# Kernel tuning notes

Hardware: AMD Instinct MI355X
Metric: run time of the kernel (lower is better)

Reference implementation:

```python
import jax, jax.numpy as jnp
import numpy as np

BS, C_IN, CTX, TGT = 2, 8, 1024, 96
D_MODEL, N_HEADS, D_FF, N_LAYERS = 256, 16, 1024, 4
PF, SF, PC, SC = 8, 4, 32, 16
NF = (CTX + SF - PF) // SF + 1   # 256 fine patches (incl. end-pad)
NC = (CTX + SC - PC) // SC + 1   # 64 coarse patches
TOTAL = NF + NC                  # 320
EPS = 1e-5
DK = D_MODEL // N_HEADS
SCALE = DK ** -0.5


def _patchify(z, plen, stride):
    # ReplicationPad1d((0, stride)) then unfold -> (bs, c, n_patches, plen)
    pad = jnp.broadcast_to(z[..., -1:], z.shape[:-1] + (stride,))
    zp = jnp.concatenate([z, pad], axis=-1)
    n = (zp.shape[-1] - plen) // stride + 1
    idx = np.arange(n)[:, None] * stride + np.arange(plen)[None, :]
    return zp[..., idx]


def _layernorm(x, s, b):
    m = x.mean(-1, keepdims=True)
    v = jnp.var(x, axis=-1, keepdims=True)
    return (x - m) * jax.lax.rsqrt(v + EPS) * s + b


def setup_inputs() -> dict:
    key = jax.random.key(0)
    ks = jax.random.split(key, 16)
    g = lambda k, shape: jax.random.normal(k, shape, jnp.float32) * 0.02
    return {
        "z": jax.random.normal(ks[0], (BS, C_IN, CTX), jnp.float32),
        "revin_w": jnp.ones((C_IN,), jnp.float32),
        "revin_b": jnp.zeros((C_IN,), jnp.float32),
        "Wf": g(ks[1], (PF, D_MODEL)), "bf": jnp.zeros((D_MODEL,), jnp.float32),
        "Wc": g(ks[2], (PC, D_MODEL)), "bc": jnp.zeros((D_MODEL,), jnp.float32),
        "W_pos": jax.random.uniform(ks[3], (TOTAL, D_MODEL), jnp.float32, -0.02, 0.02),
        "WQ": g(ks[4], (N_LAYERS, D_MODEL, D_MODEL)), "bQ": jnp.zeros((N_LAYERS, D_MODEL), jnp.float32),
        "WK": g(ks[5], (N_LAYERS, D_MODEL, D_MODEL)), "bK": jnp.zeros((N_LAYERS, D_MODEL), jnp.float32),
        "WV": g(ks[6], (N_LAYERS, D_MODEL, D_MODEL)), "bV": jnp.zeros((N_LAYERS, D_MODEL), jnp.float32),
        "WO": g(ks[7], (N_LAYERS, D_MODEL, D_MODEL)), "bO": jnp.zeros((N_LAYERS, D_MODEL), jnp.float32),
        "ln1_s": jnp.ones((N_LAYERS, D_MODEL), jnp.float32), "ln1_b": jnp.zeros((N_LAYERS, D_MODEL), jnp.float32),
        "ln2_s": jnp.ones((N_LAYERS, D_MODEL), jnp.float32), "ln2_b": jnp.zeros((N_LAYERS, D_MODEL), jnp.float32),
        "F1": g(ks[8], (N_LAYERS, D_MODEL, D_FF)), "c1": jnp.zeros((N_LAYERS, D_FF), jnp.float32),
        "F2": g(ks[9], (N_LAYERS, D_FF, D_MODEL)), "c2": jnp.zeros((N_LAYERS, D_MODEL), jnp.float32),
        "Wh": g(ks[10], (D_MODEL * TOTAL, TGT)), "bh": jnp.zeros((TGT,), jnp.float32),
    }


def reference(z, revin_w, revin_b, Wf, bf, Wc, bc, W_pos, WQ, bQ, WK, bK, WV, bV,
              WO, bO, ln1_s, ln1_b, ln2_s, ln2_b, F1, c1, F2, c2, Wh, bh):
    # RevIN norm over the time axis (last axis of (bs, c, T))
    mean = z.mean(-1, keepdims=True)
    std = jnp.sqrt(jnp.var(z, axis=-1, keepdims=True) + EPS)
    zn = (z - mean) / std * revin_w[None, :, None] + revin_b[None, :, None]

    # dual-scale patch embedding
    x_fine = _patchify(zn, PF, SF) @ Wf + bf      # (bs, c, NF, d)
    x_coarse = _patchify(zn, PC, SC) @ Wc + bc    # (bs, c, NC, d)
    x = jnp.concatenate([x_fine, x_coarse], axis=2)  # (bs, c, TOTAL, d)

    u = x.reshape(BS * C_IN, TOTAL, D_MODEL) + W_pos  # (B, S, d), B=bs*c

    # residual-score transformer encoder (post-norm)
    prev = None
    for l in range(N_LAYERS):
        q = (u @ WQ[l] + bQ[l]).reshape(-1, TOTAL, N_HEADS, DK).transpose(0, 2, 1, 3)
        k = (u @ WK[l] + bK[l]).reshape(-1, TOTAL, N_HEADS, DK).transpose(0, 2, 1, 3)
        v = (u @ WV[l] + bV[l]).reshape(-1, TOTAL, N_HEADS, DK).transpose(0, 2, 1, 3)
        s = jnp.einsum('bhqd,bhkd->bhqk', q, k) * SCALE
        if prev is not None:
            s = s + prev
        w = jax.nn.softmax(s, axis=-1)
        o = jnp.einsum('bhqk,bhkd->bhqd', w, v).transpose(0, 2, 1, 3).reshape(-1, TOTAL, D_MODEL)
        o = o @ WO[l] + bO[l]
        u = _layernorm(u + o, ln1_s[l], ln1_b[l])
        h = jax.nn.gelu(u @ F1[l] + c1[l], approximate=False) @ F2[l] + c2[l]
        u = _layernorm(u + h, ln2_s[l], ln2_b[l])
        prev = s

    # head: (bs, c, TOTAL, d) -> permute -> flatten(d, TOTAL) -> linear
    zz = u.reshape(BS, C_IN, TOTAL, D_MODEL).transpose(0, 1, 3, 2).reshape(BS, C_IN, D_MODEL * TOTAL)
    out = zz @ Wh + bh  # (bs, c, TGT)

    # RevIN denorm
    out = (out - revin_b[None, :, None]) / (revin_w[None, :, None] + EPS * EPS) * std + mean
    return out
```

## Files before the change

kernel.cpp:

```cpp
#include <hip/hip_runtime.h>
#include <math.h>

typedef unsigned short ushort;
typedef unsigned int uint;
typedef __attribute__((ext_vector_type(8))) short short8;
typedef __attribute__((ext_vector_type(4))) float f32x4;
typedef __attribute__((ext_vector_type(4))) ushort us4;

constexpr int BS = 2, C_IN = 8, CTX = 1024, TGT = 96;
constexpr int DM = 256, NH = 16, DFF = 1024, NL = 4;
constexpr int NF = 256, TOTAL = 320;
constexpr int NB = 16;
constexpr int DK = 16;
constexpr float EPS = 1e-5f;
constexpr float SCALE = 0.25f;
constexpr int KHEAD = DM * TOTAL;
constexpr int M = NB * TOTAL;

__device__ __forceinline__ ushort f2b(float x) {
    uint u = __float_as_uint(x);
    u += 0x7fff + ((u >> 16) & 1);
    return (ushort)(u >> 16);
}
__device__ __forceinline__ float bu2f(ushort x) { return __uint_as_float(((uint)x) << 16); }
__device__ __forceinline__ uint pack2(float a, float b) { return (uint)f2b(a) | ((uint)f2b(b) << 16); }

typedef __attribute__((address_space(3))) uint lds_u32;
typedef const __attribute__((address_space(1))) uint glb_u32;
__device__ __forceinline__ void ldst16(const void* g, void* l) {
    __builtin_amdgcn_global_load_lds((glb_u32*)g, (lds_u32*)l, 16, 0, 0);
}

#define PIPE_BARRIER() asm volatile("s_waitcnt vmcnt(0)\n\ts_barrier" ::: "memory")

__global__ __launch_bounds__(256) void k_prep(
        const float* __restrict__ WQ, const float* __restrict__ WK,
        const float* __restrict__ WV, const float* __restrict__ WO,
        const float* __restrict__ F1, const float* __restrict__ F2,
        const float* __restrict__ Wh,
        ushort* __restrict__ Wtqkv, ushort* __restrict__ WtO,
        ushort* __restrict__ Ft1, ushort* __restrict__ Ft2,
        ushort* __restrict__ WhT2,
        const float* __restrict__ z, const float* __restrict__ rw,
        const float* __restrict__ rb,
        const float* __restrict__ Wf, const float* __restrict__ bfv,
        const float* __restrict__ Wc, const float* __restrict__ bcv,
        const float* __restrict__ Wpos, ushort* __restrict__ u,
        const float* __restrict__ bhv, float* __restrict__ outp,
        float* __restrict__ scalef) {
    __shared__ __align__(16) ushort tile[64 * 98];
    __shared__ float szn[CTX];
    __shared__ float red1[4], red2[4];
    int i = blockIdx.x, tid = threadIdx.x;

    if (i < 768) {
        const float* src; ushort* dst; int lsrc, ldst_, r0, c0;
        if (i < 256) {
            int mat = i >> 4, l = mat >> 2, w = mat & 3;
            src = (w == 0 ? WQ : (w == 1 ? WK : (w == 2 ? WV : WO))) + l * 65536;
            dst = (w < 3) ? (Wtqkv + (size_t)l * 768 * 256 + w * 65536)
                          : (WtO + (size_t)l * 65536);
            lsrc = 256; ldst_ = 256; r0 = ((i >> 2) & 3) * 64; c0 = (i & 3) * 64;
        } else if (i < 512) {
            int j = i - 256, l = j >> 6, t = j & 63;
            src = F1 + (size_t)l * 262144; dst = Ft1 + (size_t)l * 262144;
            lsrc = 1024; ldst_ = 256; r0 = (t >> 4) * 64; c0 = (t & 15) * 64;
        } else {
            int j = i - 512, l = j >> 6, t = j & 63;
            src = F2 + (size_t)l * 262144; dst = Ft2 + (size_t)l * 262144;
            lsrc = 256; ldst_ = 1024; r0 = (t >> 2) * 64; c0 = (t & 3) * 64;
        }
#pragma unroll
        for (int it = 0; it < 4; it++) {
            int fid = it * 256 + tid;
            int fr = fid >> 4, fc = fid & 15;
            f32x4 v = *(const f32x4*)&src[(size_t)(r0 + fr) * lsrc + c0 + fc * 4];
            ushort* tr = &tile[fr * 66];
            tr[fc * 4 + 0] = f2b(v[0]); tr[fc * 4 + 1] = f2b(v[1]);
            tr[fc * 4 + 2] = f2b(v[2]); tr[fc * 4 + 3] = f2b(v[3]);
        }
        __syncthreads();
#pragma unroll
        for (int it = 0; it < 4; it++) {
            int sid = it * 256 + tid;
            int cr = sid >> 4, cc = sid & 15;
            us4 v = (us4){ tile[(cc * 4 + 0) * 66 + cr], tile[(cc * 4 + 1) * 66 + cr],
                           tile[(cc * 4 + 2) * 66 + cr], tile[(cc * 4 + 3) * 66 + cr] };
            *(us4*)&dst[(size_t)(c0 + cr) * ldst_ + r0 + cc * 4] = v;
        }
    } else if (i < 2048) {
        int j = i - 768;
        int pp = j >> 2, d0 = (j & 3) * 64;
#pragma unroll
        for (int it = 0; it < 6; it++) {
            int fid = it * 256 + tid;
            int fr = fid / 24, fc = fid % 24;
            f32x4 v = *(const f32x4*)&Wh[((size_t)(d0 + fr) * 320 + pp) * 96 + fc * 4];
            ushort* tr = &tile[fr * 98];
            tr[fc * 4 + 0] = f2b(v[0]); tr[fc * 4 + 1] = f2b(v[1]);
            tr[fc * 4 + 2] = f2b(v[2]); tr[fc * 4 + 3] = f2b(v[3]);
        }
        __syncthreads();
#pragma unroll
        for (int it = 0; it < 6; it++) {
            int sid = it * 256 + tid;
            int tr = sid >> 4, dc = sid & 15;
            us4 v = (us4){ tile[(dc * 4 + 0) * 98 + tr], tile[(dc * 4 + 1) * 98 + tr],
                           tile[(dc * 4 + 2) * 98 + tr], tile[(dc * 4 + 3) * 98 + tr] };
            *(us4*)&WhT2[(size_t)tr * KHEAD + pp * 256 + d0 + dc * 4] = v;
        }
    } else {
        int j = i - 2048;
        int bc = j / 80, pb = j % 80;
        int wave = tid >> 6, lane = tid & 63;
        f32x4 zv = *(const f32x4*)&z[bc * CTX + tid * 4];
        float s1 = zv[0] + zv[1] + zv[2] + zv[3];
        float s2 = zv[0] * zv[0] + zv[1] * zv[1] + zv[2] * zv[2] + zv[3] * zv[3];
#pragma unroll
        for (int off = 1; off < 64; off <<= 1) {
            s1 += __shfl_xor(s1, off);
            s2 += __shfl_xor(s2, off);
        }
        if (lane == 0) { red1[wave] = s1; red2[wave] = s2; }
        __syncthreads();
        s1 = red1[0] + red1[1] + red1[2] + red1[3];
        s2 = red2[0] + red2[1] + red2[2] + red2[3];
        float m = s1 * (1.0f / CTX);
        float var = s2 * (1.0f / CTX) - m * m;
        float sd = sqrtf(var + EPS);
        int c = bc & 7;
        float w = rw[c], bb = rb[c];
        float inv_sd_w = w / sd;
#pragma unroll
        for (int k = 0; k < 4; k++) szn[tid * 4 + k] = (zv[k] - m) * inv_sd_w + bb;
        if (pb == 0) {
            if (tid < TGT) outp[bc * TGT + tid] = (bhv[tid] - bb) / (w + EPS * EPS) * sd + m;
            if (tid == 0) scalef[bc] = sd / (w + EPS * EPS);
        }
        __syncthreads();
#pragma unroll
        for (int pi = 0; pi < 4; pi++) {
            int p = pb * 4 + pi, d = tid;
            float acc;
            if (p < NF) {
                acc = bfv[d];
                int base = p * 4;
#pragma unroll
                for (int q = 0; q < 8; q++)
                    acc += szn[min(base + q, CTX - 1)] * Wf[q * DM + d];
            } else {
                acc = bcv[d];
                int base = (p - NF) * 16;
#pragma unroll
                for (int q = 0; q < 32; q++)
                    acc += szn[min(base + q, CTX - 1)] * Wc[q * DM + d];
            }
            acc += Wpos[p * DM + d];
            u[((size_t)bc * TOTAL + p) * DM + d] = f2b(acc);
        }
    }
}

template <int GELU, int QKV>
__global__ __launch_bounds__(256) void k_gemm_mfma(const ushort* __restrict__ A,
                                                   const ushort* __restrict__ Wt,
                                                   const float* __restrict__ b0,
                                                   const float* __restrict__ b1,
                                                   const float* __restrict__ b2,
                                                   ushort* __restrict__ C,
                                                   ushort* __restrict__ C2,
                                                   int Mm, int N, int K) {
    __shared__ ushort As[2][64][32];
    __shared__ ushort Bs[2][64][32];
    int tid = threadIdx.x;
    int wave = tid >> 6, lane = tid & 63;
    int quad = lane >> 4, l16 = lane & 15;
    int m0 = blockIdx.y * 64, n0 = blockIdx.x * 64;

    f32x4 acc[4];
#pragma unroll
    for (int nt = 0; nt < 4; nt++) acc[nt] = (f32x4){0.f, 0.f, 0.f, 0.f};

    int srow = wave * 16 + (lane >> 2);
    int sc = (lane & 3) ^ ((srow >> 1) & 3);
    const ushort* Ag = &A[(size_t)(m0 + srow) * K + sc * 8];
    const ushort* Bg = &Wt[(size_t)(n0 + srow) * K + sc * 8];
    int rchunk = (quad ^ ((l16 >> 1) & 3)) * 8;

    ldst16(Ag, &As[0][wave * 16][0]);
    ldst16(Bg, &Bs[0][wave * 16][0]);
    PIPE_BARRIER();

    int nstep = K >> 5;
    int cur = 0;
    for (int t = 0; t < nstep; t++) {
        if (t + 1 < nstep) {
            ldst16(Ag + (t + 1) * 32, &As[cur ^ 1][wave * 16][0]);
            ldst16(Bg + (t + 1) * 32, &Bs[cur ^ 1][wave * 16][0]);
        }
        short8 af = *(const short8*)&As[cur][wave * 16 + l16][rchunk];
#pragma unroll
        for (int nt = 0; nt < 4; nt++) {
            short8 bf = *(const short8*)&Bs[cur][nt * 16 + l16][rchunk];
            acc[nt] = __builtin_amdgcn_mfma_f32_16x16x32_bf16(af, bf, acc[nt], 0, 0, 0);
        }
        PIPE_BARRIER();
        cur ^= 1;
    }
#pragma unroll
    for (int nt = 0; nt < 4; nt++) {
        int col = n0 + nt * 16 + l16;
        float bi;
        if (QKV) {
            int bs = (n0 + nt * 16) >> 8;
            const float* bp = bs == 0 ? b0 : (bs == 1 ? b1 : b2);
            bi = bp[col & 255];
        } else {
            bi = b0[col];
        }
#pragma unroll
        for (int r = 0; r < 4; r++) {
            int rowm = m0 + wave * 16 + quad * 4 + r;
            float vv = acc[nt][r] + bi;
            if (GELU) vv = vv * 0.5f * (1.0f + erff(vv * 0.70710678118f));
            if (QKV) {
                int bs = col >> 8;
                int c = col & 255, hh = c >> 4, d = c & 15;
                int bb = rowm / 320, j = rowm - bb * 320;
                size_t plane = (size_t)hh * (M * DK) + (size_t)bb * (TOTAL * DK);
                if (bs == 0) {
                    C[plane + (size_t)j * DK + d] = f2b(vv);
                } else if (bs == 1) {
                    int off = (((j >> 4) * 2 + (d >> 3)) * 16 + (j & 15)) * 8 + (d & 7);
                    C[(size_t)M * DM + plane + off] = f2b(vv);
                } else {
                    int off = ((j >> 5) * 4 + ((j & 15) >> 2)) * 128 +
                              (((j >> 4) & 1) << 2) + (j & 3) + d * 8;
                    C2[plane + off] = f2b(vv);
                }
            } else {
                C[(size_t)rowm * N + col] = f2b(vv);
            }
        }
    }
}

__global__ __launch_bounds__(256) void k_block(const ushort* __restrict__ ax,
                                               const ushort* __restrict__ WtO,
                                               const float* __restrict__ bO,
                                               const float* __restrict__ ln1s,
                                               const float* __restrict__ ln1b,
                                               const ushort* __restrict__ F1t,
                                               const ushort* __restrict__ F2t,
                                               const float* __restrict__ c1v,
                                               const float* __restrict__ c2v,
                                               const float* __restrict__ ln2s,
                                               const float* __restrict__ ln2b,
                                               ushort* __restrict__ u) {
    __shared__ ushort As[2][16][32];
    __shared__ ushort Bs[2][256][32];
    __shared__ __align__(16) ushort Au[16][264];
    __shared__ __align__(16) ushort Hs[16][264];
    __shared__ float ps1[16][4], ps2[16][4];
    int tid = threadIdx.x;
    int wave = tid >> 6, lane = tid & 63;
    int quad = lane >> 4, l16 = lane & 15;
    int m0 = blockIdx.x * 16;

    int brow = wave * 16 + (lane >> 2);
    int bsw = (lane & 3) ^ ((brow >> 1) & 3);
    int ar = lane >> 2;
    int ac = (lane & 3) ^ ((ar >> 1) & 3);
    int rchunk = (quad ^ ((l16 >> 1) & 3)) * 8;

    {
        f32x4 acc[4];
#pragma unroll
        for (int nt = 0; nt < 4; nt++) acc[nt] = (f32x4){0.f, 0.f, 0.f, 0.f};
        const ushort* Ag = &ax[(size_t)(m0 + ar) * 256 + ac * 8];
        const ushort* Bg = &WtO[(size_t)brow * 256 + bsw * 8];

        if (tid < 64) ldst16(Ag, &As[0][0][0]);
#pragma unroll
        for (int i = 0; i < 4; i++) ldst16(Bg + (size_t)i * 64 * 256, &Bs[0][i * 64 + wave * 16][0]);
        PIPE_BARRIER();
        int cur = 0;
        for (int t = 0; t < 8; t++) {
            if (t + 1 < 8) {
                if (tid < 64) ldst16(Ag + (t + 1) * 32, &As[cur ^ 1][0][0]);
#pragma unroll
                for (int i = 0; i < 4; i++)
                    ldst16(Bg + (size_t)i * 64 * 256 + (t + 1) * 32, &Bs[cur ^ 1][i * 64 + wave * 16][0]);
            }
            short8 af = *(const short8*)&As[cur][l16][rchunk];
#pragma unroll
            for (int nt = 0; nt < 4; nt++) {
                short8 bf = *(const short8*)&Bs[cur][wave * 64 + nt * 16 + l16][rchunk];
                acc[nt] = __builtin_amdgcn_mfma_f32_16x16x32_bf16(af, bf, acc[nt], 0, 0, 0);
            }
            PIPE_BARRIER();
            cur ^= 1;
        }
        float xv[4][4];
#pragma unroll
        for (int r = 0; r < 4; r++) {
            int rowg = m0 + quad * 4 + r;
            float s1 = 0.f, s2 = 0.f;
#pragma unroll
            for (int nt = 0; nt < 4; nt++) {
                int col = wave * 64 + nt * 16 + l16;
                float x = acc[nt][r] + bO[col] + bu2f(u[(size_t)rowg * DM + col]);
                xv[r][nt] = x; s1 += x; s2 += x * x;
            }
            s1 += __shfl_xor(s1, 1); s2 += __shfl_xor(s2, 1);
            s1 += __shfl_xor(s1, 2); s2 += __shfl_xor(s2, 2);
            s1 += __shfl_xor(s1, 4); s2 += __shfl_xor(s2, 4);
            s1 += __shfl_xor(s1, 8); s2 += __shfl_xor(s2, 8);
            if (l16 == 0) { ps1[quad * 4 + r][wave] = s1; ps2[quad * 4 + r][wave] = s2; }
        }
        __syncthreads();
#pragma unroll
        for (int r = 0; r < 4; r++) {
            int rowl = quad * 4 + r;
            float s1 = ps1[rowl][0] + ps1[rowl][1] + ps1[rowl][2] + ps1[rowl][3];
            float s2 = ps2[rowl][0] + ps2[rowl][1] + ps2[rowl][2] + ps2[rowl][3];
            float m = s1 * (1.0f / DM);
            float var = s2 * (1.0f / DM) - m * m;
            float rs = rsqrtf(var + EPS);
#pragma unroll
            for (int nt = 0; nt < 4; nt++) {
                int col = wave * 64 + nt * 16 + l16;
                int k32 = col >> 5, pp = (col >> 3) & 3, e = col & 7;
                int pphys = pp ^ ((rowl >> 1) & 3);
                Au[rowl][k32 * 32 + pphys * 8 + e] =
                    f2b((xv[r][nt] - m) * rs * ln1s[col] + ln1b[col]);
            }
        }
        __syncthreads();
    }

    f32x4 acc2[4];
#pragma unroll
    for (int nt = 0; nt < 4; nt++) acc2[nt] = (f32x4){0.f, 0.f, 0.f, 0.f};

    for (int c = 0; c < 4; c++) {
        f32x4 acc1[4];
#pragma unroll
        for (int nt = 0; nt < 4; nt++) acc1[nt] = (f32x4){0.f, 0.f, 0.f, 0.f};
        const ushort* Bg1 = &F1t[(size_t)(c * 256 + brow) * 256 + bsw * 8];
#pragma unroll
        for (int i = 0; i < 4; i++) ldst16(Bg1 + (size_t)i * 64 * 256, &Bs[0][i * 64 + wave * 16][0]);
        PIPE_BARRIER();
        int cur = 0;
        for (int t = 0; t < 8; t++) {
            if (t + 1 < 8) {
#pragma unroll
                for (int i = 0; i < 4; i++)
                    ldst16(Bg1 + (size_t)i * 64 * 256 + (t + 1) * 32, &Bs[cur ^ 1][i * 64 + wave * 16][0]);
            }
            short8 af = *(const short8*)&Au[l16][t * 32 + rchunk];
#pragma unroll
            for (int nt = 0; nt < 4; nt++) {
                short8 bf = *(const short8*)&Bs[cur][wave * 64 + nt * 16 + l16][rchunk];
                acc1[nt] = __builtin_amdgcn_mfma_f32_16x16x32_bf16(af, bf, acc1[nt], 0, 0, 0);
            }
            PIPE_BARRIER();
            cur ^= 1;
        }
#pragma unroll
        for (int nt = 0; nt < 4; nt++) {
            int cc = wave * 64 + nt * 16 + l16;
            float bi = c1v[c * 256 + cc];
            int k32 = cc >> 5, pp = (cc >> 3) & 3, e = cc & 7;
#pragma unroll
            for (int r = 0; r < 4; r++) {
                int row = quad * 4 + r;
                float vv = acc1[nt][r] + bi;
                vv = vv * 0.5f * (1.0f + erff(vv * 0.70710678118f));
                int pphys = pp ^ ((row >> 1) & 3);
                Hs[row][k32 * 32 + pphys * 8 + e] = f2b(vv);
            }
        }
        __syncthreads();
        const ushort* Bg2 = &F2t[(size_t)brow * 1024 + c * 256 + bsw * 8];
#pragma unroll
        for (int i = 0; i < 4; i++) ldst16(Bg2 + (size_t)i * 64 * 1024, &Bs[0][i * 64 + wave * 16][0]);
        PIPE_BARRIER();
        cur = 0;
        for (int t = 0; t < 8; t++) {
            if (t + 1 < 8) {
#pragma unroll
                for (int i = 0; i < 4; i++)
                    ldst16(Bg2 + (size_t)i * 64 * 1024 + (t + 1) * 32, &Bs[cur ^ 1][i * 64 + wave * 16][0]);
            }
            short8 af = *(const short8*)&Hs[l16][t * 32 + rchunk];
#pragma unroll
            for (int nt = 0; nt < 4; nt++) {
                short8 bf = *(const short8*)&Bs[cur][wave * 64 + nt * 16 + l16][rchunk];
                acc2[nt] = __builtin_amdgcn_mfma_f32_16x16x32_bf16(af, bf, acc2[nt], 0, 0, 0);
            }
            PIPE_BARRIER();
            cur ^= 1;
        }
    }

    float xv[4][4];
#pragma unroll
    for (int r = 0; r < 4; r++) {
        int rowl = quad * 4 + r;
        float s1 = 0.f, s2 = 0.f;
#pragma unroll
        for (int nt = 0; nt < 4; nt++) {
            int col = wave * 64 + nt * 16 + l16;
            int k32 = col >> 5, pp = (col >> 3) & 3, e = col & 7;
            int pphys = pp ^ ((rowl >> 1) & 3);
            float x = acc2[nt][r] + c2v[col] + bu2f(Au[rowl][k32 * 32 + pphys * 8 + e]);
            xv[r][nt] = x; s1 += x; s2 += x * x;
        }
        s1 += __shfl_xor(s1, 1); s2 += __shfl_xor(s2, 1);
        s1 += __shfl_xor(s1, 2); s2 += __shfl_xor(s2, 2);
        s1 += __shfl_xor(s1, 4); s2 += __shfl_xor(s2, 4);
        s1 += __shfl_xor(s1, 8); s2 += __shfl_xor(s2, 8);
        if (l16 == 0) { ps1[rowl][wave] = s1; ps2[rowl][wave] = s2; }
    }
    __syncthreads();
#pragma unroll
    for (int r = 0; r < 4; r++) {
        int rowl = quad * 4 + r, rowg = m0 + rowl;
        float s1 = ps1[rowl][0] + ps1[rowl][1] + ps1[rowl][2] + ps1[rowl][3];
        float s2 = ps2[rowl][0] + ps2[rowl][1] + ps2[rowl][2] + ps2[rowl][3];
        float m = s1 * (1.0f / DM);
        float var = s2 * (1.0f / DM) - m * m;
        float rs = rsqrtf(var + EPS);
#pragma unroll
        for (int nt = 0; nt < 4; nt++) {
            int col = wave * 64 + nt * 16 + l16;
            u[(size_t)rowg * DM + col] = f2b((xv[r][nt] - m) * rs * ln2s[col] + ln2b[col]);
        }
    }
}

__global__ __launch_bounds__(256, 3) void k_attn(const ushort* __restrict__ qk, const ushort* __restrict__ vm,
                                                 ushort* __restrict__ ao, int nj) {
    __shared__ __align__(16) ushort sh[25600];
    int bh = blockIdx.x, b = bh >> 4, h = bh & 15;
    int i0 = blockIdx.y * 64;
    int t = threadIdx.x, wave = t >> 6, lane = t & 63, quad = lane >> 4, l16 = lane & 15;
    const short8 zero8 = (short8){0, 0, 0, 0, 0, 0, 0, 0};
    size_t hplane = (size_t)h * (M * DK) + (size_t)b * (TOTAL * DK);

    int nchunks = (nj + 1) * 10;
    for (int c = wave; c < nchunks; c += 4) {
        int s = c / 10, cc = c - s * 10;
        const ushort* src = (s < nj)
            ? qk + (size_t)(2 * s + 1) * (M * DM) + hplane + cc * 512
            : vm + hplane + cc * 512;
        int dstbase = (s < nj ? s * 5120 : 20480) + cc * 512;
        ldst16(src + lane * 8, &sh[dstbase]);
    }
    short8 qfr[4] = { zero8, zero8, zero8, zero8 };
    int qrow = i0 + wave * 16 + l16;
#pragma unroll
    for (int jl = 0; jl < 4; jl++)
        if (jl < nj && quad < 2)
            qfr[jl] = *(const short8*)&qk[(size_t)(2 * jl) * (M * DM) + hplane +
                                          (size_t)qrow * DK + quad * 8];
    PIPE_BARRIER();

    f32x4 acc[20];
#pragma unroll
    for (int nt = 0; nt < 20; nt++) acc[nt] = (f32x4){0.f, 0.f, 0.f, 0.f};

    __builtin_amdgcn_s_setprio(1);
#pragma unroll
    for (int jl = 0; jl < 4; jl++) {
        if (jl < nj) {
            int kb = jl * 5120;
#pragma unroll
            for (int nt = 0; nt < 20; nt++) {
                short8 kf = *(const short8*)&sh[kb + ((nt * 2 + (quad & 1)) * 16 + l16) * 8];
                acc[nt] = __builtin_amdgcn_mfma_f32_16x16x32_bf16(kf, qfr[jl], acc[nt], 0, 0, 0);
            }
        }
    }
    __builtin_amdgcn_s_setprio(0);

    float mx = -1e30f;
#pragma unroll
    for (int nt = 0; nt < 20; nt++)
#pragma unroll
        for (int r = 0; r < 4; r++) { acc[nt][r] *= SCALE; mx = fmaxf(mx, acc[nt][r]); }
    mx = fmaxf(mx, __shfl_xor(mx, 16));
    mx = fmaxf(mx, __shfl_xor(mx, 32));
    float sum = 0.f;
#pragma unroll
    for (int nt = 0; nt < 20; nt++)
#pragma unroll
        for (int r = 0; r < 4; r++) { acc[nt][r] = __expf(acc[nt][r] - mx); sum += acc[nt][r]; }
    sum += __shfl_xor(sum, 16);
    sum += __shfl_xor(sum, 32);
    float inv = 1.f / sum;
#pragma unroll
    for (int nt = 0; nt < 20; nt++)
#pragma unroll
        for (int r = 0; r < 4; r++) acc[nt][r] *= inv;

    f32x4 oacc = (f32x4){0.f, 0.f, 0.f, 0.f};
    __builtin_amdgcn_s_setprio(1);
#pragma unroll
    for (int jt2 = 0; jt2 < 10; jt2++) {
        short8 vt = *(const short8*)&sh[20480 + ((jt2 * 4 + quad) * 16 + l16) * 8];
        union { short8 v; uint u[4]; } pf;
        pf.u[0] = pack2(acc[2 * jt2][0], acc[2 * jt2][1]);
        pf.u[1] = pack2(acc[2 * jt2][2], acc[2 * jt2][3]);
        pf.u[2] = pack2(acc[2 * jt2 + 1][0], acc[2 * jt2 + 1][1]);
        pf.u[3] = pack2(acc[2 * jt2 + 1][2], acc[2 * jt2 + 1][3]);
        oacc = __builtin_amdgcn_mfma_f32_16x16x32_bf16(vt, pf.v, oacc, 0, 0, 0);
    }
    __builtin_amdgcn_s_setprio(0);
    us4 ov4 = (us4){f2b(oacc[0]), f2b(oacc[1]), f2b(oacc[2]), f2b(oacc[3])};
    *(us4*)&ao[((size_t)b * TOTAL + i0 + wave * 16 + l16) * DM + h * DK + quad * 4] = ov4;
}

__global__ __launch_bounds__(256) void k_head(const ushort* __restrict__ u, const ushort* __restrict__ WhT2,
                                              const float* __restrict__ scalef, float* __restrict__ out) {
    int t0 = blockIdx.x * 16;
    int wave = threadIdx.x >> 6, lane = threadIdx.x & 63;
    int quad = lane >> 4, l16 = lane & 15;
    int chunk = blockIdx.y * 4 + wave;
    int kbeg = chunk * 1024;
    f32x4 acc = (f32x4){0.f, 0.f, 0.f, 0.f};
    const ushort* za = &u[(size_t)l16 * KHEAD + quad * 8];
    const ushort* wb = &WhT2[(size_t)(t0 + l16) * KHEAD + quad * 8];
#pragma unroll 4
    for (int k = kbeg; k < kbeg + 1024; k += 32) {
        short8 af = *(const short8*)&za[k];
        short8 bf = *(const short8*)&wb[k];
        acc = __builtin_amdgcn_mfma_f32_16x16x32_bf16(af, bf, acc, 0, 0, 0);
    }
#pragma unroll
    for (int r = 0; r < 4; r++) {
        int bcr = quad * 4 + r;
        atomicAdd(&out[bcr * TGT + t0 + l16], acc[r] * scalef[bcr]);
    }
}

extern "C" void kernel_launch(void* const* d_in, const int* in_sizes, int n_in,
                              void* d_out, int out_size, void* d_ws, size_t ws_size,
                              hipStream_t stream) {
    const float* z       = (const float*)d_in[0];
    const float* revin_w = (const float*)d_in[1];
    const float* revin_b = (const float*)d_in[2];
    const float* Wf      = (const float*)d_in[3];
    const float* bfv     = (const float*)d_in[4];
    const float* Wc      = (const float*)d_in[5];
    const float* bcv     = (const float*)d_in[6];
    const float* Wpos    = (const float*)d_in[7];
    const float* WQ      = (const float*)d_in[8];
    const float* bQ      = (const float*)d_in[9];
    const float* WK      = (const float*)d_in[10];
    const float* bK      = (const float*)d_in[11];
    const float* WV      = (const float*)d_in[12];
    const float* bV      = (const float*)d_in[13];
    const float* WO      = (const float*)d_in[14];
    const float* bO      = (const float*)d_in[15];
    const float* ln1s    = (const float*)d_in[16];
    const float* ln1b    = (const float*)d_in[17];
    const float* ln2s    = (const float*)d_in[18];
    const float* ln2b    = (const float*)d_in[19];
    const float* F1      = (const float*)d_in[20];
    const float* c1      = (const float*)d_in[21];
    const float* F2      = (const float*)d_in[22];
    const float* c2      = (const float*)d_in[23];
    const float* Wh      = (const float*)d_in[24];
    const float* bh      = (const float*)d_in[25];
    float* out = (float*)d_out;

    char* p = (char*)d_ws;
    float* scalef = (float*)p;   p += 16 * 4;
    p = (char*)(((size_t)p + 255) & ~255ull);
    ushort* u     = (ushort*)p;  p += (size_t)M * DM * 2;
    ushort* qkbuf = (ushort*)p;  p += (size_t)NL * 2 * M * DM * 2;
    ushort* vbuf  = (ushort*)p;  p += (size_t)M * DM * 2;
    ushort* ax    = (ushort*)p;  p += (size_t)M * DM * 2;
    ushort* Wtqkv = (ushort*)p;  p += (size_t)NL * 768 * 256 * 2;
    ushort* WtO   = (ushort*)p;  p += (size_t)NL * 256 * 256 * 2;
    ushort* Ft1   = (ushort*)p;  p += (size_t)NL * 1024 * 256 * 2;
    ushort* Ft2   = (ushort*)p;  p += (size_t)NL * 256 * 1024 * 2;
    ushort* WhT2  = (ushort*)p;  p += (size_t)TGT * KHEAD * 2;

    k_prep<<<3328, 256, 0, stream>>>(WQ, WK, WV, WO, F1, F2, Wh,
                                     Wtqkv, WtO, Ft1, Ft2, WhT2,
                                     z, revin_w, revin_b,
                                     Wf, bfv, Wc, bcv, Wpos, u,
                                     bh, out, scalef);

    for (int l = 0; l < NL; l++) {
        k_gemm_mfma<0, 1><<<dim3(12, 80), 256, 0, stream>>>(
            u, Wtqkv + (size_t)l * 768 * 256, bQ + l * DM, bK + l * DM, bV + l * DM,
            qkbuf + (size_t)l * 2 * M * DM, vbuf, M, 768, 256);
        k_attn<<<dim3(NB * NH, 5), 256, 0, stream>>>(qkbuf, vbuf, ax, l + 1);
        k_block<<<M / 16, 256, 0, stream>>>(
            ax, WtO + (size_t)l * 65536, bO + l * DM, ln1s + l * DM, ln1b + l * DM,
            Ft1 + (size_t)l * 262144, Ft2 + (size_t)l * 262144,
            c1 + l * DFF, c2 + l * DM, ln2s + l * DM, ln2b + l * DM, u);
    }

    k_head<<<dim3(TGT / 16, 20), 256, 0, stream>>>(u, WhT2, scalef, out);
}
```

Baseline: 419.2 us.

## Split fused block kernel into O-proj+LN, split-K FFN halves, and LN2 reduction

The single fused kernel doing the O projection, LN1, the full FFN and LN2 per 16-row tile is split into three kernels. The O-proj+LN1 kernel writes u1, the FFN kernel runs two blocks per row tile (each covering half of D_FF) and writes fp32 partial sums, and a small kernel adds the partials plus bias and residual and applies LN2. This doubles the grid for the FFN stage (320 to 640 blocks) to raise CU occupancy. The cost is two extra launches and an fp32 partial buffer round trip through global memory.

```diff
diff --git a/kernel.cpp b/kernel.cpp
--- a/kernel.cpp
+++ b/kernel.cpp
@@ -245,183 +245,73 @@
     }
 }
 
-__global__ __launch_bounds__(256) void k_block(const ushort* __restrict__ ax,
-                                               const ushort* __restrict__ WtO,
-                                               const float* __restrict__ bO,
-                                               const float* __restrict__ ln1s,
-                                               const float* __restrict__ ln1b,
-                                               const ushort* __restrict__ F1t,
-                                               const ushort* __restrict__ F2t,
-                                               const float* __restrict__ c1v,
-                                               const float* __restrict__ c2v,
-                                               const float* __restrict__ ln2s,
-                                               const float* __restrict__ ln2b,
-                                               ushort* __restrict__ u) {
+__global__ __launch_bounds__(256) void k_gemm_ln16(const ushort* __restrict__ A,
+                                                   const ushort* __restrict__ Wt,
+                                                   const float* __restrict__ bias,
+                                                   const float* __restrict__ ls,
+                                                   const float* __restrict__ lb,
+                                                   const ushort* __restrict__ ures,
+                                                   ushort* __restrict__ uout, int K) {
     __shared__ ushort As[2][16][32];
     __shared__ ushort Bs[2][256][32];
-    __shared__ __align__(16) ushort Au[16][264];
-    __shared__ __align__(16) ushort Hs[16][264];
     __shared__ float ps1[16][4], ps2[16][4];
     int tid = threadIdx.x;
     int wave = tid >> 6, lane = tid & 63;
     int quad = lane >> 4, l16 = lane & 15;
     int m0 = blockIdx.x * 16;
 
+    f32x4 acc[4];
+#pragma unroll
+    for (int nt = 0; nt < 4; nt++) acc[nt] = (f32x4){0.f, 0.f, 0.f, 0.f};
+
     int brow = wave * 16 + (lane >> 2);
-    int bsw = (lane & 3) ^ ((brow >> 1) & 3);
+    int bc_swz = (lane & 3) ^ ((brow >> 1) & 3);
+    const ushort* Bg0 = &Wt[(size_t)brow * K + bc_swz * 8];
     int ar = lane >> 2;
     int ac = (lane & 3) ^ ((ar >> 1) & 3);
+    const ushort* Ag = &A[(size_t)(m0 + ar) * K + ac * 8];
     int rchunk = (quad ^ ((l16 >> 1) & 3)) * 8;
 
-    {
-        f32x4 acc[4];
-#pragma unroll
-        for (int nt = 0; nt < 4; nt++) acc[nt] = (f32x4){0.f, 0.f, 0.f, 0.f};
-        const ushort* Ag = &ax[(size_t)(m0 + ar) * 256 + ac * 8];
-        const ushort* Bg = &WtO[(size_t)brow * 256 + bsw * 8];
-
-        if (tid < 64) ldst16(Ag, &As[0][0][0]);
-#pragma unroll
-        for (int i = 0; i < 4; i++) ldst16(Bg + (size_t)i * 64 * 256, &Bs[0][i * 64 + wave * 16][0]);
+    if (tid < 64) ldst16(Ag, &As[0][0][0]);
+#pragma unroll
+    for (int i = 0; i < 4; i++)
+        ldst16(Bg0 + (size_t)i * 64 * K, &Bs[0][i * 64 + wave * 16][0]);
+    PIPE_BARRIER();
+
+    int nstep = K >> 5;
+    int cur = 0;
+    for (int t = 0; t < nstep; t++) {
+        if (t + 1 < nstep) {
+            if (tid < 64) ldst16(Ag + (t + 1) * 32, &As[cur ^ 1][0][0]);
+#pragma unroll
+            for (int i = 0; i < 4; i++)
+                ldst16(Bg0 + (size_t)i * 64 * K + (t + 1) * 32, &Bs[cur ^ 1][i * 64 + wave * 16][0]);
+        }
+        short8 af = *(const short8*)&As[cur][l16][rchunk];
+#pragma unroll
+        for (int nt = 0; nt < 4; nt++) {
+            short8 bf = *(const short8*)&Bs[cur][wave * 64 + nt * 16 + l16][rchunk];
+            acc[nt] = __builtin_amdgcn_mfma_f32_16x16x32_bf16(af, bf, acc[nt], 0, 0, 0);
+        }
         PIPE_BARRIER();
-        int cur = 0;
-        for (int t = 0; t < 8; t++) {
-            if (t + 1 < 8) {
-                if (tid < 64) ldst16(Ag + (t + 1) * 32, &As[cur ^ 1][0][0]);
-#pragma unroll
-                for (int i = 0; i < 4; i++)
-                    ldst16(Bg + (size_t)i * 64 * 256 + (t + 1) * 32, &Bs[cur ^ 1][i * 64 + wave * 16][0]);
-            }
-            short8 af = *(const short8*)&As[cur][l16][rchunk];
-#pragma unroll
-            for (int nt = 0; nt < 4; nt++) {
-                short8 bf = *(const short8*)&Bs[cur][wave * 64 + nt * 16 + l16][rchunk];
-                acc[nt] = __builtin_amdgcn_mfma_f32_16x16x32_bf16(af, bf, acc[nt], 0, 0, 0);
-            }
-            PIPE_BARRIER();
-            cur ^= 1;
-        }
-        float xv[4][4];
-#pragma unroll
-        for (int r = 0; r < 4; r++) {
-            int rowg = m0 + quad * 4 + r;
-            float s1 = 0.f, s2 = 0.f;
-#pragma unroll
-            for (int nt = 0; nt < 4; nt++) {
-                int col = wave * 64 + nt * 16 + l16;
-                float x = acc[nt][r] + bO[col] + bu2f(u[(size_t)rowg * DM + col]);
-                xv[r][nt] = x; s1 += x; s2 += x * x;
-            }
-            s1 += __shfl_xor(s1, 1); s2 += __shfl_xor(s2, 1);
-            s1 += __shfl_xor(s1, 2); s2 += __shfl_xor(s2, 2);
-            s1 += __shfl_xor(s1, 4); s2 += __shfl_xor(s2, 4);
-            s1 += __shfl_xor(s1, 8); s2 += __shfl_xor(s2, 8);
-            if (l16 == 0) { ps1[quad * 4 + r][wave] = s1; ps2[quad * 4 + r][wave] = s2; }
-        }
-        __syncthreads();
-#pragma unroll
-        for (int r = 0; r < 4; r++) {
-            int rowl = quad * 4 + r;
-            float s1 = ps1[rowl][0] + ps1[rowl][1] + ps1[rowl][2] + ps1[rowl][3];
-            float s2 = ps2[rowl][0] + ps2[rowl][1] + ps2[rowl][2] + ps2[rowl][3];
-            float m = s1 * (1.0f / DM);
-            float var = s2 * (1.0f / DM) - m * m;
-            float rs = rsqrtf(var + EPS);
-#pragma unroll
-            for (int nt = 0; nt < 4; nt++) {
-                int col = wave * 64 + nt * 16 + l16;
-                int k32 = col >> 5, pp = (col >> 3) & 3, e = col & 7;
-                int pphys = pp ^ ((rowl >> 1) & 3);
-                Au[rowl][k32 * 32 + pphys * 8 + e] =
-                    f2b((xv[r][nt] - m) * rs * ln1s[col] + ln1b[col]);
-            }
-        }
-        __syncthreads();
-    }
-
-    f32x4 acc2[4];
-#pragma unroll
-    for (int nt = 0; nt < 4; nt++) acc2[nt] = (f32x4){0.f, 0.f, 0.f, 0.f};
-
-    for (int c = 0; c < 4; c++) {
-        f32x4 acc1[4];
-#pragma unroll
-        for (int nt = 0; nt < 4; nt++) acc1[nt] = (f32x4){0.f, 0.f, 0.f, 0.f};
-        const ushort* Bg1 = &F1t[(size_t)(c * 256 + brow) * 256 + bsw * 8];
-#pragma unroll
-        for (int i = 0; i < 4; i++) ldst16(Bg1 + (size_t)i * 64 * 256, &Bs[0][i * 64 + wave * 16][0]);
-        PIPE_BARRIER();
-        int cur = 0;
-        for (int t = 0; t < 8; t++) {
-            if (t + 1 < 8) {
-#pragma unroll
-                for (int i = 0; i < 4; i++)
-                    ldst16(Bg1 + (size_t)i * 64 * 256 + (t + 1) * 32, &Bs[cur ^ 1][i * 64 + wave * 16][0]);
-            }
-            short8 af = *(const short8*)&Au[l16][t * 32 + rchunk];
-#pragma unroll
-            for (int nt = 0; nt < 4; nt++) {
-                short8 bf = *(const short8*)&Bs[cur][wave * 64 + nt * 16 + l16][rchunk];
-                acc1[nt] = __builtin_amdgcn_mfma_f32_16x16x32_bf16(af, bf, acc1[nt], 0, 0, 0);
-            }
-            PIPE_BARRIER();
-            cur ^= 1;
-        }
-#pragma unroll
-        for (int nt = 0; nt < 4; nt++) {
-            int cc = wave * 64 + nt * 16 + l16;
-            float bi = c1v[c * 256 + cc];
-            int k32 = cc >> 5, pp = (cc >> 3) & 3, e = cc & 7;
-#pragma unroll
-            for (int r = 0; r < 4; r++) {
-                int row = quad * 4 + r;
-                float vv = acc1[nt][r] + bi;
-                vv = vv * 0.5f * (1.0f + erff(vv * 0.70710678118f));
-                int pphys = pp ^ ((row >> 1) & 3);
-                Hs[row][k32 * 32 + pphys * 8 + e] = f2b(vv);
-            }
-        }
-        __syncthreads();
-        const ushort* Bg2 = &F2t[(size_t)brow * 1024 + c * 256 + bsw * 8];
-#pragma unroll
-        for (int i = 0; i < 4; i++) ldst16(Bg2 + (size_t)i * 64 * 1024, &Bs[0][i * 64 + wave * 16][0]);
-        PIPE_BARRIER();
-        cur = 0;
-        for (int t = 0; t < 8; t++) {
-            if (t + 1 < 8) {
-#pragma unroll
-                for (int i = 0; i < 4; i++)
-                    ldst16(Bg2 + (size_t)i * 64 * 1024 + (t + 1) * 32, &Bs[cur ^ 1][i * 64 + wave * 16][0]);
-            }
-            short8 af = *(const short8*)&Hs[l16][t * 32 + rchunk];
-#pragma unroll
-            for (int nt = 0; nt < 4; nt++) {
-                short8 bf = *(const short8*)&Bs[cur][wave * 64 + nt * 16 + l16][rchunk];
-                acc2[nt] = __builtin_amdgcn_mfma_f32_16x16x32_bf16(af, bf, acc2[nt], 0, 0, 0);
-            }
-            PIPE_BARRIER();
-            cur ^= 1;
-        }
-    }
-
+        cur ^= 1;
+    }
     float xv[4][4];
 #pragma unroll
     for (int r = 0; r < 4; r++) {
-        int rowl = quad * 4 + r;
+        int rowg = m0 + quad * 4 + r;
         float s1 = 0.f, s2 = 0.f;
 #pragma unroll
         for (int nt = 0; nt < 4; nt++) {
             int col = wave * 64 + nt * 16 + l16;
-            int k32 = col >> 5, pp = (col >> 3) & 3, e = col & 7;
-            int pphys = pp ^ ((rowl >> 1) & 3);
-            float x = acc2[nt][r] + c2v[col] + bu2f(Au[rowl][k32 * 32 + pphys * 8 + e]);
+            float x = acc[nt][r] + bias[col] + bu2f(ures[(size_t)rowg * DM + col]);
             xv[r][nt] = x; s1 += x; s2 += x * x;
         }
         s1 += __shfl_xor(s1, 1); s2 += __shfl_xor(s2, 1);
         s1 += __shfl_xor(s1, 2); s2 += __shfl_xor(s2, 2);
         s1 += __shfl_xor(s1, 4); s2 += __shfl_xor(s2, 4);
         s1 += __shfl_xor(s1, 8); s2 += __shfl_xor(s2, 8);
-        if (l16 == 0) { ps1[rowl][wave] = s1; ps2[rowl][wave] = s2; }
+        if (l16 == 0) { ps1[quad * 4 + r][wave] = s1; ps2[quad * 4 + r][wave] = s2; }
     }
     __syncthreads();
 #pragma unroll
@@ -435,8 +325,153 @@
 #pragma unroll
         for (int nt = 0; nt < 4; nt++) {
             int col = wave * 64 + nt * 16 + l16;
-            u[(size_t)rowg * DM + col] = f2b((xv[r][nt] - m) * rs * ln2s[col] + ln2b[col]);
-        }
+            uout[(size_t)rowg * DM + col] = f2b((xv[r][nt] - m) * rs * ls[col] + lb[col]);
+        }
+    }
+}
+
+__global__ __launch_bounds__(256) void k_ffnh(const ushort* __restrict__ u1,
+                                              const ushort* __restrict__ F1t,
+                                              const ushort* __restrict__ F2t,
+                                              const float* __restrict__ c1v,
+                                              float* __restrict__ part) {
+    __shared__ __align__(16) ushort Au[16 * 256];
+    __shared__ ushort Bs[2][256][32];
+    __shared__ __align__(16) ushort Hs[16][264];
+    int tid = threadIdx.x;
+    int wave = tid >> 6, lane = tid & 63;
+    int quad = lane >> 4, l16 = lane & 15;
+    int m0 = blockIdx.x * 16;
+    int half = blockIdx.y;
+
+    int brow = wave * 16 + (lane >> 2);
+    int bsw = (lane & 3) ^ ((brow >> 1) & 3);
+    int rchunk = (quad ^ ((l16 >> 1) & 3)) * 8;
+
+    {
+        int rloc = lane >> 5, k32 = (lane & 31) >> 2, pphys = lane & 3;
+#pragma unroll
+        for (int s = 0; s < 2; s++) {
+            int ci = wave + s * 4;
+            int row = 2 * ci + rloc;
+            int plog = pphys ^ ((row >> 1) & 3);
+            ldst16(&u1[(size_t)(m0 + row) * 256 + k32 * 32 + plog * 8], &Au[ci * 512]);
+        }
+    }
+    PIPE_BARRIER();
+
+    f32x4 acc2[4];
+#pragma unroll
+    for (int nt = 0; nt < 4; nt++) acc2[nt] = (f32x4){0.f, 0.f, 0.f, 0.f};
+
+    for (int ci = 0; ci < 2; ci++) {
+        int c = half * 2 + ci;
+        f32x4 acc1[4];
+#pragma unroll
+        for (int nt = 0; nt < 4; nt++) acc1[nt] = (f32x4){0.f, 0.f, 0.f, 0.f};
+        const ushort* Bg1 = &F1t[(size_t)(c * 256 + brow) * 256 + bsw * 8];
+#pragma unroll
+        for (int i = 0; i < 4; i++) ldst16(Bg1 + (size_t)i * 64 * 256, &Bs[0][i * 64 + wave * 16][0]);
+        PIPE_BARRIER();
+        int cur = 0;
+        for (int t = 0; t < 8; t++) {
+            if (t + 1 < 8) {
+#pragma unroll
+                for (int i = 0; i < 4; i++)
+                    ldst16(Bg1 + (size_t)i * 64 * 256 + (t + 1) * 32, &Bs[cur ^ 1][i * 64 + wave * 16][0]);
+            }
+            short8 af = *(const short8*)&Au[l16 * 256 + t * 32 + rchunk];
+#pragma unroll
+            for (int nt = 0; nt < 4; nt++) {
+                short8 bf = *(const short8*)&Bs[cur][wave * 64 + nt * 16 + l16][rchunk];
+                acc1[nt] = __builtin_amdgcn_mfma_f32_16x16x32_bf16(af, bf, acc1[nt], 0, 0, 0);
+            }
+            PIPE_BARRIER();
+            cur ^= 1;
+        }
+#pragma unroll
+        for (int nt = 0; nt < 4; nt++) {
+            int cc = wave * 64 + nt * 16 + l16;
+            float bi = c1v[c * 256 + cc];
+            int k32 = cc >> 5, pp = (cc >> 3) & 3, e = cc & 7;
+#pragma unroll
+            for (int r = 0; r < 4; r++) {
+                int row = quad * 4 + r;
+                float vv = acc1[nt][r] + bi;
+                vv = vv * 0.5f * (1.0f + erff(vv * 0.70710678118f));
+                int pphys = pp ^ ((row >> 1) & 3);
+                Hs[row][k32 * 32 + pphys * 8 + e] = f2b(vv);
+            }
+        }
+        __syncthreads();
+        const ushort* Bg2 = &F2t[(size_t)brow * 1024 + c * 256 + bsw * 8];
+#pragma unroll
+        for (int i = 0; i < 4; i++) ldst16(Bg2 + (size_t)i * 64 * 1024, &Bs[0][i * 64 + wave * 16][0]);
+        PIPE_BARRIER();
+        cur = 0;
+        for (int t = 0; t < 8; t++) {
+            if (t + 1 < 8) {
+#pragma unroll
+                for (int i = 0; i < 4; i++)
+                    ldst16(Bg2 + (size_t)i * 64 * 1024 + (t + 1) * 32, &Bs[cur ^ 1][i * 64 + wave * 16][0]);
+            }
+            short8 af = *(const short8*)&Hs[l16][t * 32 + rchunk];
+#pragma unroll
+            for (int nt = 0; nt < 4; nt++) {
+                short8 bf = *(const short8*)&Bs[cur][wave * 64 + nt * 16 + l16][rchunk];
+                acc2[nt] = __builtin_amdgcn_mfma_f32_16x16x32_bf16(af, bf, acc2[nt], 0, 0, 0);
+            }
+            PIPE_BARRIER();
+            cur ^= 1;
+        }
+    }
+
+#pragma unroll
+    for (int nt = 0; nt < 4; nt++) {
+        int col = wave * 64 + nt * 16 + l16;
+#pragma unroll
+        for (int r = 0; r < 4; r++) {
+            int rowg = m0 + quad * 4 + r;
+            part[((size_t)half * M + rowg) * 256 + col] = acc2[nt][r];
+        }
+    }
+}
+
+__global__ __launch_bounds__(256) void k_ln2red(const float* __restrict__ part,
+                                                const float* __restrict__ c2v,
+                                                const ushort* __restrict__ u1,
+                                                const float* __restrict__ ls,
+                                                const float* __restrict__ lb,
+                                                ushort* __restrict__ u) {
+    int tid = threadIdx.x;
+    int wave = tid >> 6, lane = tid & 63;
+    int m0 = blockIdx.x * 16;
+#pragma unroll
+    for (int r = 0; r < 4; r++) {
+        int row = m0 + wave * 4 + r;
+        f32x4 a = *(const f32x4*)&part[(size_t)row * 256 + lane * 4];
+        f32x4 b = *(const f32x4*)&part[(size_t)(M + row) * 256 + lane * 4];
+        us4 ur = *(const us4*)&u1[(size_t)row * 256 + lane * 4];
+        float x[4];
+        float s1 = 0.f, s2 = 0.f;
+#pragma unroll
+        for (int j = 0; j < 4; j++) {
+            x[j] = a[j] + b[j] + c2v[lane * 4 + j] + bu2f(ur[j]);
+            s1 += x[j]; s2 += x[j] * x[j];
+        }
+#pragma unroll
+        for (int off = 1; off < 64; off <<= 1) {
+            s1 += __shfl_xor(s1, off);
+            s2 += __shfl_xor(s2, off);
+        }
+        float m = s1 * (1.0f / DM);
+        float var = s2 * (1.0f / DM) - m * m;
+        float rs = rsqrtf(var + EPS);
+        us4 o;
+#pragma unroll
+        for (int j = 0; j < 4; j++)
+            o[j] = f2b((x[j] - m) * rs * ls[lane * 4 + j] + lb[lane * 4 + j]);
+        *(us4*)&u[(size_t)row * 256 + lane * 4] = o;
     }
 }
 
@@ -580,9 +615,11 @@
     float* scalef = (float*)p;   p += 16 * 4;
     p = (char*)(((size_t)p + 255) & ~255ull);
     ushort* u     = (ushort*)p;  p += (size_t)M * DM * 2;
+    ushort* u1    = (ushort*)p;  p += (size_t)M * DM * 2;
     ushort* qkbuf = (ushort*)p;  p += (size_t)NL * 2 * M * DM * 2;
     ushort* vbuf  = (ushort*)p;  p += (size_t)M * DM * 2;
     ushort* ax    = (ushort*)p;  p += (size_t)M * DM * 2;
+    float* part   = (float*)p;   p += (size_t)2 * M * 256 * 4;
     ushort* Wtqkv = (ushort*)p;  p += (size_t)NL * 768 * 256 * 2;
     ushort* WtO   = (ushort*)p;  p += (size_t)NL * 256 * 256 * 2;
     ushort* Ft1   = (ushort*)p;  p += (size_t)NL * 1024 * 256 * 2;
@@ -600,10 +637,13 @@
             u, Wtqkv + (size_t)l * 768 * 256, bQ + l * DM, bK + l * DM, bV + l * DM,
             qkbuf + (size_t)l * 2 * M * DM, vbuf, M, 768, 256);
         k_attn<<<dim3(NB * NH, 5), 256, 0, stream>>>(qkbuf, vbuf, ax, l + 1);
-        k_block<<<M / 16, 256, 0, stream>>>(
+        k_gemm_ln16<<<M / 16, 256, 0, stream>>>(
             ax, WtO + (size_t)l * 65536, bO + l * DM, ln1s + l * DM, ln1b + l * DM,
-            Ft1 + (size_t)l * 262144, Ft2 + (size_t)l * 262144,
-            c1 + l * DFF, c2 + l * DM, ln2s + l * DM, ln2b + l * DM, u);
+            u, u1, 256);
+        k_ffnh<<<dim3(M / 16, 2), 256, 0, stream>>>(
+            u1, Ft1 + (size_t)l * 262144, Ft2 + (size_t)l * 262144, c1 + l * DFF, part);
+        k_ln2red<<<M / 16, 256, 0, stream>>>(
+            part, c2 + l * DM, u1, ln2s + l * DM, ln2b + l * DM, u);
     }
 
     k_head<<<dim3(TGT / 16, 20), 256, 0, stream>>>(u, WhT2, scalef, out);
```

Result: faster. 409.6 us (-2.3%).
